# Optimization experiments

Measured on AMD Instinct MI355X. Metric: run time of the kernel, lower is better.

## Reference

```python
import jax, jax.numpy as jnp
import numpy as np
import math

B, S, D, L = 16, 512, 512, 5
H = 1
DK = D // H
FF = 2 * D
VOCAB = 30
REL_VOCAB = 301  # max_relative_1d_positions + 1
SPAN = 10        # attention_span_list[0]; loop index bug keeps it fixed for all layers
EPS = 1e-5


def setup_inputs() -> dict:
    key = jax.random.key(0)
    ks = jax.random.split(key, 20)
    s = 0.02
    inp = {
        "x": jax.random.randint(ks[0], (B, S), 0, VOCAB, dtype=jnp.int64),
        "tok_emb": jax.random.normal(ks[1], (VOCAB, D), jnp.float32) * s,
        "rel_emb": jax.random.normal(ks[2], (REL_VOCAB, D), jnp.float32) * s,
        "Wq": jax.random.normal(ks[3], (L, D, D), jnp.float32) * s,
        "bq": jnp.zeros((L, D), jnp.float32),
        "Wk": jax.random.normal(ks[4], (L, D, D), jnp.float32) * s,
        "bk": jnp.zeros((L, D), jnp.float32),
        "Wv": jax.random.normal(ks[5], (L, D, D), jnp.float32) * s,
        "bv": jnp.zeros((L, D), jnp.float32),
        "Wo": jax.random.normal(ks[6], (L, D, D), jnp.float32) * s,
        "bo": jnp.zeros((L, D), jnp.float32),
        "W1": jax.random.normal(ks[7], (L, D, FF), jnp.float32) * s,
        "b1": jnp.zeros((L, FF), jnp.float32),
        "W2": jax.random.normal(ks[8], (L, FF, D), jnp.float32) * s,
        "b2": jnp.zeros((L, D), jnp.float32),
        "ln1_g": jnp.ones((L, D), jnp.float32),
        "ln1_b": jnp.zeros((L, D), jnp.float32),
        "ln2_g": jnp.ones((L, D), jnp.float32),
        "ln2_b": jnp.zeros((L, D), jnp.float32),
    }
    return inp


def _layernorm(h, g, b):
    mu = jnp.mean(h, axis=-1, keepdims=True)
    var = jnp.mean((h - mu) ** 2, axis=-1, keepdims=True)
    return (h - mu) * jax.lax.rsqrt(var + EPS) * g + b


def reference(x, tok_emb, rel_emb, Wq, bq, Wk, bk, Wv, bv, Wo, bo,
              W1, b1, W2, b2, ln1_g, ln1_b, ln2_g, ln2_b):
    seq_len = x.shape[1]
    scale = 1.0 / math.sqrt(DK)

    # relative-position bias matrix, shared by all layers (span bug in original)
    r = jnp.arange(seq_len)
    dist = jnp.clip(jnp.abs(r[None, :] - r[:, None]), 0, SPAN)  # [S,S]
    rel = rel_emb[dist]  # [S,S,D]

    causal = jnp.tril(jnp.ones((seq_len, seq_len), dtype=bool))  # [S,S]

    h = tok_emb[x]  # [B,S,D]
    for l in range(L):
        q = h @ Wq[l] + bq[l]  # [B,S,D]
        k = h @ Wk[l] + bk[l]
        v = h @ Wv[l] + bv[l]
        # heads=1: [B,S,D] acts as [B,H=1,S,DK]
        score1 = jnp.einsum('bid,bjd->bij', q, k) * scale
        score2 = jnp.einsum('bid,ijd->bij', q, rel)
        # NOTE: original divides (score1 + score2) by sqrt(d_k) again
        scores = (score1 + score2) * scale
        scores = jnp.where(causal[None, :, :], scores, -1e9)
        p = jax.nn.softmax(scores, axis=-1)
        ctx = jnp.einsum('bij,bjd->bid', p, v)
        x_att = ctx @ Wo[l] + bo[l]
        h = _layernorm(h + x_att, ln1_g[l], ln1_b[l])
        ff = jax.nn.relu(h @ W1[l] + b1[l]) @ W2[l] + b2[l]
        h = _layernorm(h + ff, ln2_g[l], ln2_b[l])
    return h
```

## Files before the change

kernel.cpp:

```cpp
#include <hip/hip_runtime.h>
#include <math.h>

#define S 512
#define D 512
#define FFD 1024
#define NB 16
#define NL 5

typedef __attribute__((ext_vector_type(8))) short bf16x8;
typedef __attribute__((ext_vector_type(4))) float f32x4;

__device__ __forceinline__ short f2bf(float f){
  union { float f; unsigned u; } c; c.f = f;
  unsigned r = c.u + 0x7FFFu + ((c.u >> 16) & 1u);
  return (short)(r >> 16);
}
__device__ __forceinline__ float bf2f(short s){
  union { unsigned u; float f; } c; c.u = ((unsigned)(unsigned short)s) << 16;
  return c.f;
}

__device__ __forceinline__ void gload16(const void* g, void* l){
  __builtin_amdgcn_global_load_lds(
      (const __attribute__((address_space(1))) void*)g,
      (__attribute__((address_space(3))) void*)l, 16, 0, 0);
}

__device__ __forceinline__ float wsum(float v){
  #pragma unroll
  for (int o = 32; o; o >>= 1) v += __shfl_down(v, o, 64);
  return v;
}

__global__ __launch_bounds__(256) void embed_k(const int* __restrict__ x,
    const float* __restrict__ tok, short* __restrict__ hb){
  int idx = blockIdx.x * 256 + threadIdx.x;
  int row = idx >> 9;
  int d   = idx & 511;
  hb[idx] = f2bf(tok[x[row] * D + d]);
}

__global__ __launch_bounds__(256) void bcat_k(const float* __restrict__ bq,
    const float* __restrict__ bk, const float* __restrict__ bv,
    const float* __restrict__ rel, float* __restrict__ out){
  int i = blockIdx.x * 256 + threadIdx.x;
  if (i >= NL * 1664) return;
  int lay = i / 1664, c = i % 1664;
  float v;
  if      (c <  512) v = bq[lay * 512 + c];
  else if (c < 1024) v = bk[lay * 512 + c - 512];
  else if (c < 1536) v = bv[lay * 512 + c - 1024];
  else if (c < 1547){
    int cc = c - 1536;
    float s = 0.f;
    for (int j = 0; j < 512; j++) s += bq[lay * 512 + j] * rel[cc * 512 + j];
    v = s;
  } else v = 0.f;
  out[i] = v;
}

__global__ __launch_bounds__(256) void wrel_k(
    const float* __restrict__ Wq, const float* __restrict__ rel,
    short* __restrict__ WqkvT){
  const int bid = blockIdx.x;
  const int lay = bid >> 7, kc = bid & 127;
  const int w = threadIdx.x >> 6, lane = threadIdx.x & 63;
  const int k = kc * 4 + w;
  const float* wrow = Wq + (size_t)lay * 262144 + (size_t)k * 512 + lane * 8;
  float qv[8];
  #pragma unroll
  for (int e = 0; e < 8; e++) qv[e] = wrow[e];
  short* dst = WqkvT + (size_t)lay * 851968;
  #pragma unroll
  for (int c = 0; c < 11; c++){
    const float* rp = rel + c * 512 + lane * 8;
    float s = 0.f;
    #pragma unroll
    for (int e = 0; e < 8; e++) s = fmaf(qv[e], rp[e], s);
    s = wsum(s);
    if (lane == 0) dst[(size_t)(1536 + c) * 512 + k] = f2bf(s);
  }
  if (lane == 0){
    #pragma unroll
    for (int c = 11; c < 16; c++) dst[(size_t)(1536 + c) * 512 + k] = 0;
  }
}

__global__ __launch_bounds__(256) void wtrans_k(
    const float* __restrict__ Wq, const float* __restrict__ Wk,
    const float* __restrict__ Wv, const float* __restrict__ Wo,
    const float* __restrict__ W1, const float* __restrict__ W2,
    short* __restrict__ WqkvT, short* __restrict__ WoT,
    short* __restrict__ W1T, short* __restrict__ W2T)
{
  __shared__ float tl[64][65];
  int id = blockIdx.x;
  const float* src; short* dst; int K, N, tk, tn;
  if (id < 1280){
    int mat = id / 320, r = id % 320, lay = r / 64, tt = r % 64;
    tk = tt >> 3; tn = tt & 7; K = 512; N = 512;
    const float* s;
    short* d;
    if (mat == 0){ s = Wq; d = WqkvT + (size_t)lay * 851968; }
    else if (mat == 1){ s = Wk; d = WqkvT + (size_t)lay * 851968 + 262144; }
    else if (mat == 2){ s = Wv; d = WqkvT + (size_t)lay * 851968 + 524288; }
    else { s = Wo; d = WoT + (size_t)lay * 262144; }
    src = s + (size_t)lay * 262144; dst = d;
  } else if (id < 1920){
    int r = id - 1280, lay = r / 128, tt = r % 128;
    tk = tt >> 4; tn = tt & 15; K = 512; N = 1024;
    src = W1 + (size_t)lay * 524288; dst = W1T + (size_t)lay * 524288;
  } else {
    int r = id - 1920, lay = r / 128, tt = r % 128;
    tk = tt >> 3; tn = tt & 7; K = 1024; N = 512;
    src = W2 + (size_t)lay * 524288; dst = W2T + (size_t)lay * 524288;
  }
  const int k0 = tk * 64, n0 = tn * 64;
  const int t = threadIdx.x;
  const int lr = t >> 4, lc = (t & 15) * 4;
  #pragma unroll
  for (int s = 0; s < 4; s++){
    int row = lr + s * 16;
    float4 v = *(const float4*)&src[(size_t)(k0 + row) * N + n0 + lc];
    tl[row][lc + 0] = v.x; tl[row][lc + 1] = v.y;
    tl[row][lc + 2] = v.z; tl[row][lc + 3] = v.w;
  }
  __syncthreads();
  const int nr8 = t >> 3, kc8 = (t & 7) * 8;
  #pragma unroll
  for (int s = 0; s < 2; s++){
    int nr = nr8 + s * 32;
    bf16x8 o;
    #pragma unroll
    for (int e = 0; e < 8; e++) o[e] = f2bf(tl[kc8 + e][nr]);
    *(bf16x8*)&dst[(size_t)(n0 + nr) * K + k0 + kc8] = o;
  }
}

template<int ROWS, int PAN>
__device__ __forceinline__ void stage_tile(const short* __restrict__ G, int ld,
                                           int kbase, char* ldsBase, int w, int l){
  constexpr int CALLS = ROWS * PAN / 64;
  #pragma unroll
  for (int c = 0; c < CALLS; c++){
    const int idx = w * CALLS + c;
    const int panel = idx / (ROWS / 16);
    const int chunk = idx % (ROWS / 16);
    const short* src = G + (size_t)(chunk * 16 + (l >> 2)) * ld
                         + kbase + panel * 32 + (l & 3) * 8;
    gload16(src, ldsBase + idx * 1024);
  }
}

template<int BM, int BN, int MODE, int BK>
__global__ __launch_bounds__(256) void mm_nt(
    const short* __restrict__ A, int ldA,
    const short* __restrict__ B, int ldB,
    const float* __restrict__ bias, void* __restrict__ C, int ldC,
    const float* __restrict__ qrel, short* __restrict__ vT,
    float* __restrict__ qrelOut,
    int K, long batA, long batB, long batC)
{
  constexpr int PAN = BK / 32;
  constexpr int STAGE_SH = 2 * BK * (BM + BN);
  constexpr int BOUNCE_SH = BM * BN;
  constexpr int TB_ST = BM + 8;
  constexpr int TBOUNCE_SH = (MODE == 5) ? BN * TB_ST : 0;
  constexpr int SMEM_A = STAGE_SH > BOUNCE_SH ? STAGE_SH : BOUNCE_SH;
  constexpr int SMEM_SH = SMEM_A > TBOUNCE_SH ? SMEM_A : TBOUNCE_SH;
  __shared__ short smem[SMEM_SH];
  short* As = smem;
  short* Bs = smem + 2 * BM * BK;

  const int gx = gridDim.x, gy = gridDim.y;
  int flat = ((int)blockIdx.z * gy + (int)blockIdx.y) * gx + (int)blockIdx.x;
  const int nwg = gx * gy * (int)gridDim.z;
  const int chunk = nwg >> 3;
  flat = (flat & 7) * chunk + (flat >> 3);
  const int bx = flat % gx;
  const int byy = (flat / gx) % gy;
  const int b = flat / (gx * gy);

  const int m0 = byy * BM, n0 = bx * BN;
  if (MODE == 3 && n0 >= m0 + BM) return;
  int nk = K / BK;
  if (MODE == 4){ int km = (m0 + BM) / BK; nk = km < nk ? km : nk; }

  constexpr int FM = BM / 32, FN = BN / 32;
  f32x4 acc[FM][FN];
  const f32x4 z = {0.f, 0.f, 0.f, 0.f};
  #pragma unroll
  for (int m = 0; m < FM; m++)
    #pragma unroll
    for (int n = 0; n < FN; n++) acc[m][n] = z;

  const int t = threadIdx.x, l = t & 63, w = t >> 6;
  const short* Ag = A + (size_t)b * batA + (size_t)m0 * ldA;
  const short* Bg = B + (size_t)b * batB + (size_t)n0 * ldB;

  stage_tile<BM, PAN>(Ag, ldA, 0, (char*)As, w, l);
  stage_tile<BN, PAN>(Bg, ldB, 0, (char*)Bs, w, l);
  __syncthreads();

  const int wm = (w >> 1) * (BM / 2), wn = (w & 1) * (BN / 2);
  const int kc = (l >> 4) * 8;
  float rs[FM];
  #pragma unroll
  for (int m = 0; m < FM; m++) rs[m] = 0.f;

  for (int ks = 0; ks < nk; ks++){
    const int cur = ks & 1;
    if (ks + 1 < nk){
      const int nxt = cur ^ 1;
      stage_tile<BM, PAN>(Ag, ldA, (ks + 1) * BK, (char*)As + nxt * (BM * BK * 2), w, l);
      stage_tile<BN, PAN>(Bg, ldB, (ks + 1) * BK, (char*)Bs + nxt * (BN * BK * 2), w, l);
    }
    const short* Ab = As + cur * (BM * BK);
    const short* Bb = Bs + cur * (BN * BK);
    #pragma unroll
    for (int p = 0; p < PAN; p++){
      bf16x8 af[FM], bfr[FN];
      #pragma unroll
      for (int m = 0; m < FM; m++)
        af[m] = *(const bf16x8*)&Ab[p * BM * 32 + (wm + m * 16 + (l & 15)) * 32 + kc];
      #pragma unroll
      for (int n = 0; n < FN; n++)
        bfr[n] = *(const bf16x8*)&Bb[p * BN * 32 + (wn + n * 16 + (l & 15)) * 32 + kc];
      if (MODE == 4){
        #pragma unroll
        for (int m = 0; m < FM; m++){
          float s = 0.f;
          #pragma unroll
          for (int e = 0; e < 8; e++) s += bf2f(af[m][e]);
          rs[m] += s;
        }
      }
      #pragma unroll
      for (int m = 0; m < FM; m++)
        #pragma unroll
        for (int n = 0; n < FN; n++)
          acc[m][n] = __builtin_amdgcn_mfma_f32_16x16x32_bf16(af[m], bfr[n], acc[m][n], 0, 0, 0);
    }
    __syncthreads();
  }

  float invr[FM][4];
  if (MODE == 4){
    #pragma unroll
    for (int m = 0; m < FM; m++){
      float r = rs[m];
      r += __shfl_xor(r, 16, 64);
      r += __shfl_xor(r, 32, 64);
      #pragma unroll
      for (int rr = 0; rr < 4; rr++)
        invr[m][rr] = 1.0f / __shfl(r, (l >> 4) * 4 + rr, 64);
    }
  }

  const size_t cbase = (size_t)b * batC;

  if (MODE == 5 && n0 >= 1024){
    if (n0 < 1536){
      short* tb = smem;
      #pragma unroll
      for (int m = 0; m < FM; m++){
        const int rb = wm + m * 16 + (l >> 4) * 4;
        #pragma unroll
        for (int n = 0; n < FN; n++){
          const int cl = wn + n * 16 + (l & 15);
          const int col = n0 + cl;
          union { short s[4]; uint2 u; } tmp;
          #pragma unroll
          for (int r = 0; r < 4; r++) tmp.s[r] = f2bf(acc[m][n][r] + bias[col]);
          *(uint2*)&tb[cl * TB_ST + rb] = tmp.u;
        }
      }
      __syncthreads();
      const int dbase = n0 - 1024;
      constexpr int ITER_T = BM * BN / 2048;
      #pragma unroll
      for (int c = 0; c < ITER_T; c++){
        const int idx = c * 2048 + t * 8;
        const int dl = idx / BM, sl = idx % BM;
        const int grow = m0 + sl;
        const int bb = grow >> 9, s0 = grow & 511;
        *(bf16x8*)&vT[(size_t)bb * 262144 + (size_t)(dbase + dl) * 512 + s0] =
            *(const bf16x8*)&tb[dl * TB_ST + sl];
      }
      return;
    } else {
      #pragma unroll
      for (int m = 0; m < FM; m++){
        const int rbase = m0 + wm + m * 16 + (l >> 4) * 4;
        #pragma unroll
        for (int n = 0; n < FN; n++){
          const int col = n0 + wn + n * 16 + (l & 15);
          if (col < 1552){
            const int c = col - 1536;
            #pragma unroll
            for (int r = 0; r < 4; r++)
              qrelOut[(size_t)(rbase + r) * 16 + c] = acc[m][n][r] + bias[col];
          }
        }
      }
      return;
    }
  }

  #pragma unroll
  for (int m = 0; m < FM; m++){
    const int rb = wm + m * 16 + (l >> 4) * 4;
    #pragma unroll
    for (int n = 0; n < FN; n++){
      const int cl = wn + n * 16 + (l & 15);
      const int col = n0 + cl;
      #pragma unroll
      for (int r = 0; r < 4; r++){
        const int row = m0 + rb + r;
        float v = acc[m][n][r];
        short ov;
        if (MODE == 3){
          if (col <= row){
            int dd = row - col; if (dd > 10) dd = 10;
            float sv = v * (1.0f / 512.0f)
                     + qrel[((size_t)b * S + row) * 16 + dd] * 0.044194173824159216f;
            ov = f2bf(__expf(sv));
          } else ov = 0;
        } else if (MODE == 4){
          ov = f2bf(v * invr[m][r]);
        } else {
          v += bias[col];
          if (MODE == 2) v = fmaxf(v, 0.f);
          ov = f2bf(v);
        }
        smem[(rb + r) * BN + cl] = ov;
      }
    }
  }
  __syncthreads();
  constexpr int ITER = BM * BN / 2048;
  #pragma unroll
  for (int c = 0; c < ITER; c++){
    const int idx = c * 2048 + t * 8;
    const int row = idx / BN, cc = idx % BN;
    *(bf16x8*)&((short*)C)[cbase + (size_t)(m0 + row) * ldC + n0 + cc] =
        *(const bf16x8*)&smem[idx];
  }
}

template<int FINAL>
__global__ __launch_bounds__(256) void add_ln_k(
    short* __restrict__ hb, const short* __restrict__ y,
    const float* __restrict__ g, const float* __restrict__ be,
    float* __restrict__ hOut)
{
  const int t = threadIdx.x, w = t >> 6, l = t & 63;
  const int row = blockIdx.x * 4 + w;
  short* hbr = hb + (size_t)row * D;
  const short* yr = y + (size_t)row * D;
  bf16x8 h8 = *(const bf16x8*)&hbr[l * 8];
  bf16x8 y8 = *(const bf16x8*)&yr[l * 8];
  float v[8], s1 = 0.f, s2 = 0.f;
  #pragma unroll
  for (int e = 0; e < 8; e++){
    v[e] = bf2f(h8[e]) + bf2f(y8[e]);
    s1 += v[e];
    s2 += v[e] * v[e];
  }
  #pragma unroll
  for (int o = 32; o; o >>= 1){
    s1 += __shfl_xor(s1, o, 64);
    s2 += __shfl_xor(s2, o, 64);
  }
  const float mu  = s1 * (1.0f / 512.0f);
  const float var = s2 * (1.0f / 512.0f) - mu * mu;
  const float rcp = rsqrtf(var + 1e-5f);
  float4 g0 = *(const float4*)&g[l * 8];
  float4 g1 = *(const float4*)&g[l * 8 + 4];
  float4 b0 = *(const float4*)&be[l * 8];
  float4 b1 = *(const float4*)&be[l * 8 + 4];
  float gv[8] = {g0.x, g0.y, g0.z, g0.w, g1.x, g1.y, g1.z, g1.w};
  float bv[8] = {b0.x, b0.y, b0.z, b0.w, b1.x, b1.y, b1.z, b1.w};
  float o[8];
  #pragma unroll
  for (int e = 0; e < 8; e++) o[e] = (v[e] - mu) * rcp * gv[e] + bv[e];
  if (FINAL){
    float* ho = hOut + (size_t)row * D + l * 8;
    *(float4*)&ho[0] = make_float4(o[0], o[1], o[2], o[3]);
    *(float4*)&ho[4] = make_float4(o[4], o[5], o[6], o[7]);
  } else {
    bf16x8 ob;
    #pragma unroll
    for (int e = 0; e < 8; e++) ob[e] = f2bf(o[e]);
    *(bf16x8*)&hbr[l * 8] = ob;
  }
}

extern "C" void kernel_launch(void* const* d_in, const int* in_sizes, int n_in,
                              void* d_out, int out_size, void* d_ws, size_t ws_size,
                              hipStream_t stream)
{
  const int*   x   = (const int*)  d_in[0];
  const float* tok = (const float*)d_in[1];
  const float* rel = (const float*)d_in[2];
  const float* Wq  = (const float*)d_in[3];  const float* bq = (const float*)d_in[4];
  const float* Wk  = (const float*)d_in[5];  const float* bk = (const float*)d_in[6];
  const float* Wv  = (const float*)d_in[7];  const float* bv = (const float*)d_in[8];
  const float* Wo  = (const float*)d_in[9];  const float* bo = (const float*)d_in[10];
  const float* W1  = (const float*)d_in[11]; const float* b1 = (const float*)d_in[12];
  const float* W2  = (const float*)d_in[13]; const float* b2 = (const float*)d_in[14];
  const float* g1  = (const float*)d_in[15]; const float* be1 = (const float*)d_in[16];
  const float* g2  = (const float*)d_in[17]; const float* be2 = (const float*)d_in[18];
  (void)in_sizes; (void)n_in; (void)out_size; (void)ws_size;

  float* h = (float*)d_out;

  char* ws = (char*)d_ws;
  const size_t MB = 1 << 20;
  short* hb     = (short*)(ws);
  short* qkv    = (short*)(ws + 8 * MB);
  short* vT     = (short*)(ws + 24 * MB);
  short* p      = (short*)(ws + 32 * MB);
  short* ctx    = (short*)(ws + 40 * MB);
  short* xatt   = (short*)(ws + 48 * MB);
  short* ffmid  = (short*)(ws + 32 * MB);
  float* qrelb  = (float*)(ws + 56 * MB);
  float* bqkv   = (float*)(ws + 56 * MB + 512 * 1024);
  short* wb     = (short*)(ws + 57 * MB);
  short* WqkvT  = wb;
  short* WoT    = WqkvT + (size_t)5 * 851968;
  short* W1T    = WoT   + (size_t)5 * 262144;
  short* W2T    = W1T   + (size_t)5 * 524288;
  short* ffout  = xatt;

  const int M = NB * S;

  wtrans_k<<<2560, 256, 0, stream>>>(Wq, Wk, Wv, Wo, W1, W2, WqkvT, WoT, W1T, W2T);
  wrel_k<<<640, 256, 0, stream>>>(Wq, rel, WqkvT);
  bcat_k<<<(NL * 1664 + 255) / 256, 256, 0, stream>>>(bq, bk, bv, rel, bqkv);
  embed_k<<<(size_t)M * D / 256, 256, 0, stream>>>(x, tok, hb);

  for (int l = 0; l < NL; l++){
    mm_nt<128, 128, 5, 32><<<dim3(13, 64, 1), 256, 0, stream>>>(
        hb, 512, WqkvT + (size_t)l * 851968, 512, bqkv + l * 1664,
        qkv, 1024, nullptr, vT, qrelb, 512, 0, 0, 0);

    mm_nt<64, 128, 3, 64><<<dim3(4, 8, NB), 256, 0, stream>>>(
        qkv, 1024, qkv + 512, 1024, nullptr,
        p, 512, qrelb, nullptr, nullptr, 512,
        (long)S * 1024, (long)S * 1024, (long)S * S);

    mm_nt<64, 128, 4, 64><<<dim3(4, 8, NB), 256, 0, stream>>>(
        p, 512, vT, 512, nullptr,
        ctx, 512, nullptr, nullptr, nullptr, 512,
        (long)S * S, (long)D * S, (long)S * D);

    mm_nt<128, 64, 1, 64><<<dim3(8, 64, 1), 256, 0, stream>>>(
        ctx, 512, WoT + (size_t)l * 262144, 512, bo + l * 512,
        xatt, 512, nullptr, nullptr, nullptr, 512, 0, 0, 0);
    add_ln_k<0><<<M / 4, 256, 0, stream>>>(hb, xatt, g1 + l * 512, be1 + l * 512, nullptr);

    mm_nt<128, 128, 2, 32><<<dim3(8, 64, 1), 256, 0, stream>>>(
        hb, 512, W1T + (size_t)l * 524288, 512, b1 + l * 1024,
        ffmid, 1024, nullptr, nullptr, nullptr, 512, 0, 0, 0);
    mm_nt<128, 64, 1, 64><<<dim3(8, 64, 1), 256, 0, stream>>>(
        ffmid, 1024, W2T + (size_t)l * 524288, 1024, b2 + l * 512,
        ffout, 512, nullptr, nullptr, nullptr, 1024, 0, 0, 0);
    if (l < NL - 1)
      add_ln_k<0><<<M / 4, 256, 0, stream>>>(hb, ffout, g2 + l * 512, be2 + l * 512, nullptr);
    else
      add_ln_k<1><<<M / 4, 256, 0, stream>>>(hb, ffout, g2 + l * 512, be2 + l * 512, h);
  }
}
```

Baseline: 538.7 us.

## Use vmcnt-based waits in GEMM pipeline and widen QKV tile to 256 columns

The GEMM main loop swaps full __syncthreads for explicit s_waitcnt vmcnt waits plus raw barriers, so the next stage's global-to-LDS loads can stay in flight while the current stage is computed. The fused QKV projection moves to a 128x256 tile, which pads the weight layout to 1792 columns with memset zeroing and writes the epilogue in two halves through a smaller LDS bounce buffer. The FFN1 GEMM also moves to BK=64. The aim is less barrier stall and better reuse of the A tile, at the cost of more register pressure and extra padded work in the QKV GEMM.

```diff
diff --git a/kernel.cpp b/kernel.cpp
--- a/kernel.cpp
+++ b/kernel.cpp
@@ -24,6 +24,17 @@
   __builtin_amdgcn_global_load_lds(
       (const __attribute__((address_space(1))) void*)g,
       (__attribute__((address_space(3))) void*)l, 16, 0, 0);
+}
+
+template<int N>
+__device__ __forceinline__ void waitcnt_vm(){
+  if      constexpr (N == 0)  asm volatile("s_waitcnt vmcnt(0)"  ::: "memory");
+  else if constexpr (N == 2)  asm volatile("s_waitcnt vmcnt(2)"  ::: "memory");
+  else if constexpr (N == 4)  asm volatile("s_waitcnt vmcnt(4)"  ::: "memory");
+  else if constexpr (N == 6)  asm volatile("s_waitcnt vmcnt(6)"  ::: "memory");
+  else if constexpr (N == 8)  asm volatile("s_waitcnt vmcnt(8)"  ::: "memory");
+  else if constexpr (N == 10) asm volatile("s_waitcnt vmcnt(10)" ::: "memory");
+  else                        asm volatile("s_waitcnt vmcnt(12)" ::: "memory");
 }
 
 __device__ __forceinline__ float wsum(float v){
@@ -44,8 +55,8 @@
     const float* __restrict__ bk, const float* __restrict__ bv,
     const float* __restrict__ rel, float* __restrict__ out){
   int i = blockIdx.x * 256 + threadIdx.x;
-  if (i >= NL * 1664) return;
-  int lay = i / 1664, c = i % 1664;
+  if (i >= NL * 1792) return;
+  int lay = i / 1792, c = i % 1792;
   float v;
   if      (c <  512) v = bq[lay * 512 + c];
   else if (c < 1024) v = bk[lay * 512 + c - 512];
@@ -70,7 +81,7 @@
   float qv[8];
   #pragma unroll
   for (int e = 0; e < 8; e++) qv[e] = wrow[e];
-  short* dst = WqkvT + (size_t)lay * 851968;
+  short* dst = WqkvT + (size_t)lay * 917504;
   #pragma unroll
   for (int c = 0; c < 11; c++){
     const float* rp = rel + c * 512 + lane * 8;
@@ -101,9 +112,9 @@
     tk = tt >> 3; tn = tt & 7; K = 512; N = 512;
     const float* s;
     short* d;
-    if (mat == 0){ s = Wq; d = WqkvT + (size_t)lay * 851968; }
-    else if (mat == 1){ s = Wk; d = WqkvT + (size_t)lay * 851968 + 262144; }
-    else if (mat == 2){ s = Wv; d = WqkvT + (size_t)lay * 851968 + 524288; }
+    if (mat == 0){ s = Wq; d = WqkvT + (size_t)lay * 917504; }
+    else if (mat == 1){ s = Wk; d = WqkvT + (size_t)lay * 917504 + 262144; }
+    else if (mat == 2){ s = Wv; d = WqkvT + (size_t)lay * 917504 + 524288; }
     else { s = Wo; d = WoT + (size_t)lay * 262144; }
     src = s + (size_t)lay * 262144; dst = d;
   } else if (id < 1920){
@@ -162,10 +173,13 @@
     int K, long batA, long batB, long batC)
 {
   constexpr int PAN = BK / 32;
+  constexpr int CT  = (BM + BN) * PAN / 64;
+  constexpr int BNH = BN > 128 ? 128 : BN;
+  constexpr int NHALF = BN / BNH;
   constexpr int STAGE_SH = 2 * BK * (BM + BN);
-  constexpr int BOUNCE_SH = BM * BN;
+  constexpr int BOUNCE_SH = BM * BNH;
   constexpr int TB_ST = BM + 8;
-  constexpr int TBOUNCE_SH = (MODE == 5) ? BN * TB_ST : 0;
+  constexpr int TBOUNCE_SH = (MODE == 5) ? BNH * TB_ST : 0;
   constexpr int SMEM_A = STAGE_SH > BOUNCE_SH ? STAGE_SH : BOUNCE_SH;
   constexpr int SMEM_SH = SMEM_A > TBOUNCE_SH ? SMEM_A : TBOUNCE_SH;
   __shared__ short smem[SMEM_SH];
@@ -200,7 +214,6 @@
 
   stage_tile<BM, PAN>(Ag, ldA, 0, (char*)As, w, l);
   stage_tile<BN, PAN>(Bg, ldB, 0, (char*)Bs, w, l);
-  __syncthreads();
 
   const int wm = (w >> 1) * (BM / 2), wn = (w & 1) * (BN / 2);
   const int kc = (l >> 4) * 8;
@@ -214,7 +227,12 @@
       const int nxt = cur ^ 1;
       stage_tile<BM, PAN>(Ag, ldA, (ks + 1) * BK, (char*)As + nxt * (BM * BK * 2), w, l);
       stage_tile<BN, PAN>(Bg, ldB, (ks + 1) * BK, (char*)Bs + nxt * (BN * BK * 2), w, l);
+      waitcnt_vm<CT>();
+    } else {
+      waitcnt_vm<0>();
     }
+    __builtin_amdgcn_s_barrier();
+    __builtin_amdgcn_sched_barrier(0);
     const short* Ab = As + cur * (BM * BK);
     const short* Bb = Bs + cur * (BN * BK);
     #pragma unroll
@@ -241,7 +259,8 @@
         for (int n = 0; n < FN; n++)
           acc[m][n] = __builtin_amdgcn_mfma_f32_16x16x32_bf16(af[m], bfr[n], acc[m][n], 0, 0, 0);
     }
-    __syncthreads();
+    __builtin_amdgcn_sched_barrier(0);
+    __builtin_amdgcn_s_barrier();
   }
 
   float invr[FM][4];
@@ -263,29 +282,36 @@
     if (n0 < 1536){
       short* tb = smem;
       #pragma unroll
-      for (int m = 0; m < FM; m++){
-        const int rb = wm + m * 16 + (l >> 4) * 4;
+      for (int nh = 0; nh < NHALF; nh++){
+        if (NHALF == 1 || (w & 1) == nh){
+          #pragma unroll
+          for (int m = 0; m < FM; m++){
+            const int rb = wm + m * 16 + (l >> 4) * 4;
+            #pragma unroll
+            for (int n = 0; n < FN; n++){
+              const int cl = wn + n * 16 + (l & 15);
+              const int col = n0 + cl;
+              const int clh = cl - nh * BNH;
+              union { short s[4]; uint2 u; } tmp;
+              #pragma unroll
+              for (int r = 0; r < 4; r++) tmp.s[r] = f2bf(acc[m][n][r] + bias[col]);
+              *(uint2*)&tb[clh * TB_ST + rb] = tmp.u;
+            }
+          }
+        }
+        __syncthreads();
+        const int dbase = n0 - 1024 + nh * BNH;
+        constexpr int ITER_T = BM * BNH / 2048;
         #pragma unroll
-        for (int n = 0; n < FN; n++){
-          const int cl = wn + n * 16 + (l & 15);
-          const int col = n0 + cl;
-          union { short s[4]; uint2 u; } tmp;
-          #pragma unroll
-          for (int r = 0; r < 4; r++) tmp.s[r] = f2bf(acc[m][n][r] + bias[col]);
-          *(uint2*)&tb[cl * TB_ST + rb] = tmp.u;
+        for (int c = 0; c < ITER_T; c++){
+          const int idx = c * 2048 + t * 8;
+          const int dl = idx / BM, sl = idx % BM;
+          const int grow = m0 + sl;
+          const int bb = grow >> 9, s0 = grow & 511;
+          *(bf16x8*)&vT[(size_t)bb * 262144 + (size_t)(dbase + dl) * 512 + s0] =
+              *(const bf16x8*)&tb[dl * TB_ST + sl];
         }
-      }
-      __syncthreads();
-      const int dbase = n0 - 1024;
-      constexpr int ITER_T = BM * BN / 2048;
-      #pragma unroll
-      for (int c = 0; c < ITER_T; c++){
-        const int idx = c * 2048 + t * 8;
-        const int dl = idx / BM, sl = idx % BM;
-        const int grow = m0 + sl;
-        const int bb = grow >> 9, s0 = grow & 511;
-        *(bf16x8*)&vT[(size_t)bb * 262144 + (size_t)(dbase + dl) * 512 + s0] =
-            *(const bf16x8*)&tb[dl * TB_ST + sl];
+        if (nh + 1 < NHALF) __syncthreads();
       }
       return;
     } else {
@@ -308,43 +334,50 @@
   }
 
   #pragma unroll
-  for (int m = 0; m < FM; m++){
-    const int rb = wm + m * 16 + (l >> 4) * 4;
-    #pragma unroll
-    for (int n = 0; n < FN; n++){
-      const int cl = wn + n * 16 + (l & 15);
-      const int col = n0 + cl;
-      #pragma unroll
-      for (int r = 0; r < 4; r++){
-        const int row = m0 + rb + r;
-        float v = acc[m][n][r];
-        short ov;
-        if (MODE == 3){
-          if (col <= row){
-            int dd = row - col; if (dd > 10) dd = 10;
-            float sv = v * (1.0f / 512.0f)
-                     + qrel[((size_t)b * S + row) * 16 + dd] * 0.044194173824159216f;
-            ov = f2bf(__expf(sv));
-          } else ov = 0;
-        } else if (MODE == 4){
-          ov = f2bf(v * invr[m][r]);
-        } else {
-          v += bias[col];
-          if (MODE == 2) v = fmaxf(v, 0.f);
-          ov = f2bf(v);
+  for (int nh = 0; nh < NHALF; nh++){
+    if (NHALF == 1 || (w & 1) == nh){
+      #pragma unroll
+      for (int m = 0; m < FM; m++){
+        const int rb = wm + m * 16 + (l >> 4) * 4;
+        #pragma unroll
+        for (int n = 0; n < FN; n++){
+          const int cl = wn + n * 16 + (l & 15);
+          const int col = n0 + cl;
+          const int clh = cl - nh * BNH;
+          #pragma unroll
+          for (int r = 0; r < 4; r++){
+            const int row = m0 + rb + r;
+            float v = acc[m][n][r];
+            short ov;
+            if (MODE == 3){
+              if (col <= row){
+                int dd = row - col; if (dd > 10) dd = 10;
+                float sv = v * (1.0f / 512.0f)
+                         + qrel[((size_t)b * S + row) * 16 + dd] * 0.044194173824159216f;
+                ov = f2bf(__expf(sv));
+              } else ov = 0;
+            } else if (MODE == 4){
+              ov = f2bf(v * invr[m][r]);
+            } else {
+              v += bias[col];
+              if (MODE == 2) v = fmaxf(v, 0.f);
+              ov = f2bf(v);
+            }
+            smem[(rb + r) * BNH + clh] = ov;
+          }
         }
-        smem[(rb + r) * BN + cl] = ov;
       }
     }
-  }
-  __syncthreads();
-  constexpr int ITER = BM * BN / 2048;
-  #pragma unroll
-  for (int c = 0; c < ITER; c++){
-    const int idx = c * 2048 + t * 8;
-    const int row = idx / BN, cc = idx % BN;
-    *(bf16x8*)&((short*)C)[cbase + (size_t)(m0 + row) * ldC + n0 + cc] =
-        *(const bf16x8*)&smem[idx];
+    __syncthreads();
+    constexpr int ITER = BM * BNH / 2048;
+    #pragma unroll
+    for (int c = 0; c < ITER; c++){
+      const int idx = c * 2048 + t * 8;
+      const int row = idx / BNH, cc = idx % BNH;
+      *(bf16x8*)&((short*)C)[cbase + (size_t)(m0 + row) * ldC + n0 + nh * BNH + cc] =
+          *(const bf16x8*)&smem[idx];
+    }
+    if (nh + 1 < NHALF) __syncthreads();
   }
 }
 
@@ -428,21 +461,24 @@
   float* bqkv   = (float*)(ws + 56 * MB + 512 * 1024);
   short* wb     = (short*)(ws + 57 * MB);
   short* WqkvT  = wb;
-  short* WoT    = WqkvT + (size_t)5 * 851968;
+  short* WoT    = WqkvT + (size_t)5 * 917504;
   short* W1T    = WoT   + (size_t)5 * 262144;
   short* W2T    = W1T   + (size_t)5 * 524288;
   short* ffout  = xatt;
 
   const int M = NB * S;
 
+  for (int l2 = 0; l2 < NL; l2++)
+    hipMemsetAsync(WqkvT + (size_t)l2 * 917504 + (size_t)1552 * 512, 0,
+                   (size_t)240 * 512 * 2, stream);
   wtrans_k<<<2560, 256, 0, stream>>>(Wq, Wk, Wv, Wo, W1, W2, WqkvT, WoT, W1T, W2T);
   wrel_k<<<640, 256, 0, stream>>>(Wq, rel, WqkvT);
-  bcat_k<<<(NL * 1664 + 255) / 256, 256, 0, stream>>>(bq, bk, bv, rel, bqkv);
+  bcat_k<<<(NL * 1792 + 255) / 256, 256, 0, stream>>>(bq, bk, bv, rel, bqkv);
   embed_k<<<(size_t)M * D / 256, 256, 0, stream>>>(x, tok, hb);
 
   for (int l = 0; l < NL; l++){
-    mm_nt<128, 128, 5, 32><<<dim3(13, 64, 1), 256, 0, stream>>>(
-        hb, 512, WqkvT + (size_t)l * 851968, 512, bqkv + l * 1664,
+    mm_nt<128, 256, 5, 32><<<dim3(7, 64, 1), 256, 0, stream>>>(
+        hb, 512, WqkvT + (size_t)l * 917504, 512, bqkv + l * 1792,
         qkv, 1024, nullptr, vT, qrelb, 512, 0, 0, 0);
 
     mm_nt<64, 128, 3, 64><<<dim3(4, 8, NB), 256, 0, stream>>>(
@@ -460,7 +496,7 @@
         xatt, 512, nullptr, nullptr, nullptr, 512, 0, 0, 0);
     add_ln_k<0><<<M / 4, 256, 0, stream>>>(hb, xatt, g1 + l * 512, be1 + l * 512, nullptr);
 
-    mm_nt<128, 128, 2, 32><<<dim3(8, 64, 1), 256, 0, stream>>>(
+    mm_nt<128, 128, 2, 64><<<dim3(8, 64, 1), 256, 0, stream>>>(
         hb, 512, W1T + (size_t)l * 524288, 512, b1 + l * 1024,
         ffmid, 1024, nullptr, nullptr, nullptr, 512, 0, 0, 0);
     mm_nt<128, 64, 1, 64><<<dim3(8, 64, 1), 256, 0, stream>>>(
```

Result: slower. 583.7 us (+8.4%).
